# Kernel tuning notes

Hardware: AMD Instinct MI355X
Metric: run time of the kernel (lower is better)

Reference implementation:

```python
import jax, jax.numpy as jnp
import numpy as np

B, C, H, W = 8, 512, 64, 64
S = 64
STD = 0.001  # torch init.normal_(weight, std=0.001)


def setup_inputs() -> dict:
    key = jax.random.key(0)
    ks = jax.random.split(key, 7)
    return {
        "queries": jax.random.normal(ks[0], (B, C, H, W), dtype=jnp.float32),
        "k": jax.random.normal(ks[1], (B, C, H, W), dtype=jnp.float32),
        "v": jax.random.normal(ks[2], (B, C, H, W), dtype=jnp.float32),
        "Wq": jax.random.normal(ks[3], (S, C), dtype=jnp.float32) * STD,
        "Wk": jax.random.normal(ks[4], (S, C), dtype=jnp.float32) * STD,
        "Wv": jax.random.normal(ks[5], (S, C), dtype=jnp.float32) * STD,
        "Wl": jax.random.normal(ks[6], (C, S), dtype=jnp.float32) * STD,
    }


def _branch(A, Bp, Cp, Wl):
    # A,Bp,Cp: [h,w,b,S] projected tensors
    m = jnp.einsum('hwbs,hwbt->hwst', A, Bp)          # [h,w,S,S]
    m = jax.nn.softmax(m, axis=1)                      # softmax over w (dim=1, as in torch)
    o = jnp.einsum('hwst,hwbt->hwsb', m, Cp)           # [h,w,S,b]
    o = o / jnp.sum(o, axis=2, keepdims=True)          # normalize over S
    o = jnp.einsum('hwsb,cs->hwbc', o, Wl)             # transpose + Linear(S->C)
    return jnp.transpose(o, (2, 3, 0, 1))              # [b,c,h,w]


def reference(queries, k, v, Wq, Wk, Wv, Wl):
    q = jnp.transpose(queries, (2, 3, 0, 1))  # [h,w,b,c]
    kk = jnp.transpose(k, (2, 3, 0, 1))
    vv = jnp.transpose(v, (2, 3, 0, 1))
    aq = jnp.einsum('hwbc,sc->hwbs', q, Wq)   # [h,w,b,S]
    ak = jnp.einsum('hwbc,sc->hwbs', kk, Wk)
    av = jnp.einsum('hwbc,sc->hwbs', vv, Wv)
    out_q = _branch(aq, ak, av, Wl)
    out_k = _branch(ak, av, aq, Wl)
    out_v = _branch(av, aq, ak, Wl)
    return jnp.concatenate((out_q, out_k, out_v), axis=0)  # [3b,c,h,w]
```

## Files before the change

kernel.cpp:

```cpp
#include <hip/hip_runtime.h>
#include <hip/hip_bf16.h>

#define HW 4096
#define CCH 512
#define SDIM 64
#define BDIM 8

typedef __attribute__((ext_vector_type(8))) short short8;
typedef __attribute__((ext_vector_type(4))) float f32x4;

static __device__ __forceinline__ ushort f2bf(float f) {
  __hip_bfloat16 h = __float2bfloat16(f);
  return *reinterpret_cast<ushort*>(&h);
}
static __device__ __forceinline__ float bf2f(ushort u) {
  union { unsigned int u32; float f; } c;
  c.u32 = ((unsigned int)u) << 16;
  return c.f;
}

static __device__ __forceinline__ void gll16(const float* g, float* lds_base) {
  __builtin_amdgcn_global_load_lds(
      (const __attribute__((address_space(1))) unsigned int*)g,
      (__attribute__((address_space(3))) unsigned int*)lds_base, 16, 0, 0);
}

__global__ __launch_bounds__(256) void prep_kernel(const float* __restrict__ Wq,
                                                   const float* __restrict__ Wk,
                                                   const float* __restrict__ Wv,
                                                   ushort* __restrict__ whi,
                                                   ushort* __restrict__ wmid,
                                                   ushort* __restrict__ wlo) {
  const float* W = blockIdx.y == 0 ? Wq : (blockIdx.y == 1 ? Wk : Wv);
  const int idx = blockIdx.x * 1024 + threadIdx.x * 4;
  float4 f = *reinterpret_cast<const float4*>(&W[idx]);
  ushort4 h, m, l;
  float r, r2;
  h.x = f2bf(f.x); r = f.x - bf2f(h.x); m.x = f2bf(r); r2 = r - bf2f(m.x); l.x = f2bf(r2);
  h.y = f2bf(f.y); r = f.y - bf2f(h.y); m.y = f2bf(r); r2 = r - bf2f(m.y); l.y = f2bf(r2);
  h.z = f2bf(f.z); r = f.z - bf2f(h.z); m.z = f2bf(r); r2 = r - bf2f(m.z); l.z = f2bf(r2);
  h.w = f2bf(f.w); r = f.w - bf2f(h.w); m.w = f2bf(r); r2 = r - bf2f(m.w); l.w = f2bf(r2);
  const size_t o = (size_t)blockIdx.y * (SDIM * CCH) + idx;
  *reinterpret_cast<ushort4*>(&whi[o])  = h;
  *reinterpret_cast<ushort4*>(&wmid[o]) = m;
  *reinterpret_cast<ushort4*>(&wlo[o])  = l;
}

__global__ __launch_bounds__(256, 2) void proj_mfma_kernel(const float* __restrict__ q,
                                                           const float* __restrict__ k,
                                                           const float* __restrict__ v,
                                                           const ushort* __restrict__ whi,
                                                           const ushort* __restrict__ wmid,
                                                           const ushort* __restrict__ wlo,
                                                           float* __restrict__ ap) {
  __shared__ float Xs[2][4][64 * 32];
  const int mt = blockIdx.x;
  const int b = blockIdx.y;
  const int br = blockIdx.z;
  const float* x = br == 0 ? q : (br == 1 ? k : v);
  const ushort* wh = whi + (size_t)br * SDIM * CCH;
  const ushort* wm = wmid + (size_t)br * SDIM * CCH;
  const ushort* wl = wlo + (size_t)br * SDIM * CCH;
  float* apo = ap + (size_t)br * HW * 512;
  const int hw0 = mt * 128;
  const int tid = threadIdx.x;
  const int l = tid & 63;
  const int wid = tid >> 6;
  const int wstrip = wid * 32;
  const int row16 = l & 15;
  const int kgrp = l >> 4;
  const float* xsrc = x + (size_t)b * CCH * HW + hw0 + wstrip + (l & 7) * 4;
  const int csub = l >> 3;

  f32x4 acc_hi[2][4] = {};
  f32x4 acc_co[2][4] = {};

#define STAGE(BUF, C0)                                                        \
  do {                                                                        \
    float* ldsb = &Xs[BUF][wid][0];                                           \
    _Pragma("unroll") for (int j = 0; j < 8; ++j)                             \
      gll16(xsrc + (size_t)((C0) + j * 8 + csub) * HW, ldsb + j * 256);       \
  } while (0)

#define COMPUTE(BUF, C0)                                                                           \
  do {                                                                                             \
    const float* lw = &Xs[BUF][wid][0];                                                            \
    _Pragma("unroll") for (int ks = 0; ks < 2; ++ks) {                                             \
      short8 bh[4], bm[4], bl[4];                                                                  \
      _Pragma("unroll") for (int nf = 0; nf < 4; ++nf) {                                           \
        const size_t off = (size_t)(nf * 16 + row16) * CCH + (C0) + ks * 32 + kgrp * 8;            \
        bh[nf] = *reinterpret_cast<const short8*>(&wh[off]);                                       \
        bm[nf] = *reinterpret_cast<const short8*>(&wm[off]);                                       \
        bl[nf] = *reinterpret_cast<const short8*>(&wl[off]);                                       \
      }                                                                                            \
      _Pragma("unroll") for (int mf = 0; mf < 2; ++mf) {                                           \
        ushort th[8], tm[8], tl[8];                                                                \
        _Pragma("unroll") for (int i = 0; i < 8; ++i) {                                            \
          const float f = lw[(ks * 32 + kgrp * 8 + i) * 32 + mf * 16 + row16];                     \
          const ushort h = f2bf(f);                                                                \
          const float r = f - bf2f(h);                                                             \
          const ushort mv = f2bf(r);                                                               \
          const float r2 = r - bf2f(mv);                                                           \
          th[i] = h; tm[i] = mv; tl[i] = f2bf(r2);                                                 \
        }                                                                                          \
        const short8 ah = *reinterpret_cast<const short8*>(th);                                    \
        const short8 am = *reinterpret_cast<const short8*>(tm);                                    \
        const short8 al = *reinterpret_cast<const short8*>(tl);                                    \
        _Pragma("unroll") for (int nf = 0; nf < 4; ++nf) {                                         \
          acc_hi[mf][nf] = __builtin_amdgcn_mfma_f32_16x16x32_bf16(ah, bh[nf], acc_hi[mf][nf], 0, 0, 0); \
          acc_co[mf][nf] = __builtin_amdgcn_mfma_f32_16x16x32_bf16(ah, bm[nf], acc_co[mf][nf], 0, 0, 0); \
          acc_co[mf][nf] = __builtin_amdgcn_mfma_f32_16x16x32_bf16(am, bh[nf], acc_co[mf][nf], 0, 0, 0); \
          acc_co[mf][nf] = __builtin_amdgcn_mfma_f32_16x16x32_bf16(am, bm[nf], acc_co[mf][nf], 0, 0, 0); \
          acc_co[mf][nf] = __builtin_amdgcn_mfma_f32_16x16x32_bf16(ah, bl[nf], acc_co[mf][nf], 0, 0, 0); \
          acc_co[mf][nf] = __builtin_amdgcn_mfma_f32_16x16x32_bf16(al, bh[nf], acc_co[mf][nf], 0, 0, 0); \
          acc_co[mf][nf] = __builtin_amdgcn_mfma_f32_16x16x32_bf16(am, bl[nf], acc_co[mf][nf], 0, 0, 0); \
          acc_co[mf][nf] = __builtin_amdgcn_mfma_f32_16x16x32_bf16(al, bm[nf], acc_co[mf][nf], 0, 0, 0); \
        }                                                                                          \
      }                                                                                            \
    }                                                                                              \
  } while (0)

  STAGE(0, 0);
#pragma unroll
  for (int cc = 0; cc < 8; ++cc) {
    if (cc < 7) STAGE((cc + 1) & 1, (cc + 1) * 64);
    __builtin_amdgcn_sched_barrier(0);
    if (cc < 7) {
      asm volatile("s_waitcnt vmcnt(8)" ::: "memory");
    } else {
      asm volatile("s_waitcnt vmcnt(0)" ::: "memory");
    }
    __builtin_amdgcn_sched_barrier(0);
    COMPUTE(cc & 1, cc * 64);
  }
#undef STAGE
#undef COMPUTE

#pragma unroll
  for (int mf = 0; mf < 2; ++mf)
#pragma unroll
    for (int nf = 0; nf < 4; ++nf)
#pragma unroll
      for (int r = 0; r < 4; ++r) {
        const int m = hw0 + wstrip + mf * 16 + kgrp * 4 + r;
        apo[(size_t)m * 512 + b * 64 + nf * 16 + row16] = acc_hi[mf][nf][r] + acc_co[mf][nf][r];
      }
}

__global__ __launch_bounds__(512) void denom_kernel(const float* __restrict__ ap,
                                                    float* __restrict__ rD) {
  __shared__ float As[8 * 16];
  __shared__ float Bs[8 * 64];
  const int h = blockIdx.x, br = blockIdx.y, sq = blockIdx.z;
  const float* A  = ap + ((size_t)br * HW + (size_t)h * 64) * (BDIM * SDIM);
  const float* Bp = ap + ((size_t)((br + 1) % 3) * HW + (size_t)h * 64) * (BDIM * SDIM);
  const int tid = threadIdx.x;
  const int t = tid & 63;
  const int sg = tid >> 6;
  float D[2] = {};
  for (int w = 0; w < 64; ++w) {
    __syncthreads();
    if (tid < 128) As[tid] = A[w * 512 + (tid >> 4) * 64 + sq * 16 + (tid & 15)];
    Bs[tid] = Bp[w * 512 + tid];
    __syncthreads();
    float bv[8];
#pragma unroll
    for (int b = 0; b < 8; ++b) bv[b] = Bs[b * 64 + t];
#pragma unroll
    for (int j = 0; j < 2; ++j) {
      const int sl = sg * 2 + j;
      float m = 0.f;
#pragma unroll
      for (int b = 0; b < 8; ++b) m = fmaf(As[b * 16 + sl], bv[b], m);
      D[j] += __expf(m);
    }
  }
#pragma unroll
  for (int j = 0; j < 2; ++j)
    rD[((size_t)(br * 64 + h) * 64 + sq * 16 + sg * 2 + j) * 64 + t] = 1.0f / D[j];
}

__global__ __launch_bounds__(256) void attn_kernel(const float* __restrict__ ap,
                                                   const float* __restrict__ rD,
                                                   float* __restrict__ on) {
  __shared__ float As[8 * 64], Bs[8 * 64], Cs[8 * 64];
  __shared__ float Ms[64 * 68];
  const int wc = blockIdx.x, h = blockIdx.y, br = blockIdx.z;
  const float* A  = ap + ((size_t)br * HW + h * 64) * 512;
  const float* Bp = ap + ((size_t)((br + 1) % 3) * HW + h * 64) * 512;
  const float* Cp = ap + ((size_t)((br + 2) % 3) * HW + h * 64) * 512;
  const float* rDp = rD + (size_t)(br * 64 + h) * 4096;
  const int tid = threadIdx.x;
  for (int w = wc * 8; w < wc * 8 + 8; ++w) {
    __syncthreads();
#pragma unroll
    for (int it = 0; it < 2; ++it) {
      int idx = it * 256 + tid;
      As[idx] = A[w * 512 + idx];
      Bs[idx] = Bp[w * 512 + idx];
      Cs[idx] = Cp[w * 512 + idx];
    }
    __syncthreads();
    {
      const int t = tid & 63, sg = tid >> 6;
      float bv[8];
#pragma unroll
      for (int b = 0; b < 8; ++b) bv[b] = Bs[b * 64 + t];
#pragma unroll
      for (int j = 0; j < 16; ++j) {
        int s = sg * 16 + j;
        float m = 0.f;
#pragma unroll
        for (int b = 0; b < 8; ++b) m = fmaf(As[b * 64 + s], bv[b], m);
        Ms[s * 68 + t] = __expf(m) * rDp[s * 64 + t];
      }
    }
    __syncthreads();
    const int s2 = tid & 63, bq = tid >> 6;
    float o0 = 0.f, o1 = 0.f;
#pragma unroll
    for (int tt = 0; tt < 64; tt += 4) {
      float4 mv = *reinterpret_cast<const float4*>(&Ms[s2 * 68 + tt]);
      float4 c0 = *reinterpret_cast<const float4*>(&Cs[bq * 64 + tt]);
      float4 c1 = *reinterpret_cast<const float4*>(&Cs[(bq + 4) * 64 + tt]);
      o0 = fmaf(mv.w, c0.w, fmaf(mv.z, c0.z, fmaf(mv.y, c0.y, fmaf(mv.x, c0.x, o0))));
      o1 = fmaf(mv.w, c1.w, fmaf(mv.z, c1.z, fmaf(mv.y, c1.y, fmaf(mv.x, c1.x, o1))));
    }
    float n0 = o0, n1 = o1;
#pragma unroll
    for (int off = 32; off > 0; off >>= 1) {
      n0 += __shfl_xor(n0, off);
      n1 += __shfl_xor(n1, off);
    }
    const float r0 = 1.0f / n0, r1 = 1.0f / n1;
    const size_t ob = ((size_t)br * HW + h * 64 + w) * 512;
    on[ob + (size_t)bq * 64 + s2] = o0 * r0;
    on[ob + (size_t)(bq + 4) * 64 + s2] = o1 * r1;
  }
}

__global__ __launch_bounds__(256) void out_kernel(const float* __restrict__ on,
                                                  const float* __restrict__ wl,
                                                  float* __restrict__ out) {
  __shared__ float Os[128 * 68];
  const int hwt = blockIdx.x;
  const int brb = blockIdx.y;
  const int br = brb >> 3, b = brb & 7;
  const int hw0 = hwt * 128;
  const int tid = threadIdx.x;
  const int l = tid & 63;
  const int wv = tid >> 6;
  const int l15 = l & 15;
  const int kgrp = l >> 4;

  {
    const int row = tid >> 4;
    const int s4 = (tid & 15) * 4;
#pragma unroll
    for (int it = 0; it < 8; ++it) {
      const int r = row + it * 16;
      *reinterpret_cast<float4*>(&Os[r * 68 + s4]) =
          *reinterpret_cast<const float4*>(&on[((size_t)(br * HW + hw0 + r) * 8 + b) * 64 + s4]);
    }
  }
  __syncthreads();

  short8 onh[2][2], onl[2][2];
#pragma unroll
  for (int nf = 0; nf < 2; ++nf)
#pragma unroll
    for (int ks = 0; ks < 2; ++ks) {
      const int row = wv * 32 + nf * 16 + l15;
      const float* p = &Os[row * 68 + ks * 32 + kgrp * 8];
      ushort th[8], tl[8];
#pragma unroll
      for (int i = 0; i < 8; ++i) {
        const float f = p[i];
        const ushort h = f2bf(f);
        th[i] = h;
        tl[i] = f2bf(f - bf2f(h));
      }
      onh[nf][ks] = *reinterpret_cast<const short8*>(th);
      onl[nf][ks] = *reinterpret_cast<const short8*>(tl);
    }

  for (int mf = 0; mf < 32; ++mf) {
    f32x4 acc[2] = {};
#pragma unroll
    for (int ks = 0; ks < 2; ++ks) {
      const float* wp = &wl[(size_t)(mf * 16 + l15) * 64 + ks * 32 + kgrp * 8];
      ushort th[8], tl[8];
#pragma unroll
      for (int i = 0; i < 8; ++i) {
        const float f = wp[i];
        const ushort h = f2bf(f);
        th[i] = h;
        tl[i] = f2bf(f - bf2f(h));
      }
      const short8 wh8 = *reinterpret_cast<const short8*>(th);
      const short8 wl8 = *reinterpret_cast<const short8*>(tl);
#pragma unroll
      for (int nf = 0; nf < 2; ++nf) {
        acc[nf] = __builtin_amdgcn_mfma_f32_16x16x32_bf16(wh8, onh[nf][ks], acc[nf], 0, 0, 0);
        acc[nf] = __builtin_amdgcn_mfma_f32_16x16x32_bf16(wh8, onl[nf][ks], acc[nf], 0, 0, 0);
        acc[nf] = __builtin_amdgcn_mfma_f32_16x16x32_bf16(wl8, onh[nf][ks], acc[nf], 0, 0, 0);
      }
    }
#pragma unroll
    for (int nf = 0; nf < 2; ++nf)
#pragma unroll
      for (int r = 0; r < 4; ++r) {
        const int cc = mf * 16 + kgrp * 4 + r;
        out[(size_t)(brb * 512 + cc) * HW + hw0 + wv * 32 + nf * 16 + l15] = acc[nf][r];
      }
  }
}

extern "C" void kernel_launch(void* const* d_in, const int* in_sizes, int n_in,
                              void* d_out, int out_size, void* d_ws, size_t ws_size,
                              hipStream_t stream) {
  const float* q  = (const float*)d_in[0];
  const float* k  = (const float*)d_in[1];
  const float* v  = (const float*)d_in[2];
  const float* Wq = (const float*)d_in[3];
  const float* Wk = (const float*)d_in[4];
  const float* Wv = (const float*)d_in[5];
  const float* Wl = (const float*)d_in[6];
  float* out = (float*)d_out;

  float* ap = (float*)d_ws;
  float* rD = ap + (size_t)3 * HW * 512;
  float* on = rD + (size_t)3 * 64 * 64 * 64;
  ushort* whi  = (ushort*)rD;
  ushort* wmid = whi + (size_t)3 * SDIM * CCH;
  ushort* wlo  = wmid + (size_t)3 * SDIM * CCH;

  prep_kernel<<<dim3(32, 3), 256, 0, stream>>>(Wq, Wk, Wv, whi, wmid, wlo);
  proj_mfma_kernel<<<dim3(32, 8, 3), 256, 0, stream>>>(q, k, v, whi, wmid, wlo, ap);
  denom_kernel<<<dim3(64, 3, 4), 512, 0, stream>>>(ap, rD);
  attn_kernel<<<dim3(8, 64, 3), 256, 0, stream>>>(ap, rD, on);
  out_kernel<<<dim3(32, 24), 256, 0, stream>>>(on, Wl, out);
}
```

Before: 283.0 us.

## Restructure projection kernel to 512-thread blocks with cooperative 32-channel staging

The projection kernel moves from 256-thread blocks, where each wave privately stages and consumes its own 32-pixel strip in 64-channel chunks, to 512-thread blocks covering 256 pixels. All eight waves now cooperatively load 32-channel slices into a shared double buffer and synchronise with block barriers. Weight fragments are loaded once per 32-channel step rather than per 64-channel chunk. The goal is fewer blocks, coalesced full-row loads and smaller per-wave register and LDS footprints, at the cost of two block-wide barriers per channel step and less latency hiding, since each wave has only one chunk in flight.

Result: slower. 329.3 us (+16.3%).

```diff
diff --git a/kernel.cpp b/kernel.cpp
--- a/kernel.cpp
+++ b/kernel.cpp
@@ -46,14 +46,14 @@
   *reinterpret_cast<ushort4*>(&wlo[o])  = l;
 }
 
-__global__ __launch_bounds__(256, 2) void proj_mfma_kernel(const float* __restrict__ q,
+__global__ __launch_bounds__(512, 2) void proj_mfma_kernel(const float* __restrict__ q,
                                                            const float* __restrict__ k,
                                                            const float* __restrict__ v,
                                                            const ushort* __restrict__ whi,
                                                            const ushort* __restrict__ wmid,
                                                            const ushort* __restrict__ wlo,
                                                            float* __restrict__ ap) {
-  __shared__ float Xs[2][4][64 * 32];
+  __shared__ float Xs[2][32 * 256];
   const int mt = blockIdx.x;
   const int b = blockIdx.y;
   const int br = blockIdx.z;
@@ -62,79 +62,79 @@
   const ushort* wm = wmid + (size_t)br * SDIM * CCH;
   const ushort* wl = wlo + (size_t)br * SDIM * CCH;
   float* apo = ap + (size_t)br * HW * 512;
-  const int hw0 = mt * 128;
+  const int hw0 = mt * 256;
   const int tid = threadIdx.x;
   const int l = tid & 63;
-  const int wid = tid >> 6;
-  const int wstrip = wid * 32;
+  const int w = tid >> 6;
+  const int w4 = w * 4;
   const int row16 = l & 15;
   const int kgrp = l >> 4;
-  const float* xsrc = x + (size_t)b * CCH * HW + hw0 + wstrip + (l & 7) * 4;
-  const int csub = l >> 3;
+  const float* xb = x + (size_t)b * CCH * HW + hw0 + l * 4;
 
   f32x4 acc_hi[2][4] = {};
   f32x4 acc_co[2][4] = {};
 
-#define STAGE(BUF, C0)                                                        \
-  do {                                                                        \
-    float* ldsb = &Xs[BUF][wid][0];                                           \
-    _Pragma("unroll") for (int j = 0; j < 8; ++j)                             \
-      gll16(xsrc + (size_t)((C0) + j * 8 + csub) * HW, ldsb + j * 256);       \
-  } while (0)
-
-#define COMPUTE(BUF, C0)                                                                           \
-  do {                                                                                             \
-    const float* lw = &Xs[BUF][wid][0];                                                            \
-    _Pragma("unroll") for (int ks = 0; ks < 2; ++ks) {                                             \
-      short8 bh[4], bm[4], bl[4];                                                                  \
-      _Pragma("unroll") for (int nf = 0; nf < 4; ++nf) {                                           \
-        const size_t off = (size_t)(nf * 16 + row16) * CCH + (C0) + ks * 32 + kgrp * 8;            \
-        bh[nf] = *reinterpret_cast<const short8*>(&wh[off]);                                       \
-        bm[nf] = *reinterpret_cast<const short8*>(&wm[off]);                                       \
-        bl[nf] = *reinterpret_cast<const short8*>(&wl[off]);                                       \
-      }                                                                                            \
-      _Pragma("unroll") for (int mf = 0; mf < 2; ++mf) {                                           \
-        ushort th[8], tm[8], tl[8];                                                                \
-        _Pragma("unroll") for (int i = 0; i < 8; ++i) {                                            \
-          const float f = lw[(ks * 32 + kgrp * 8 + i) * 32 + mf * 16 + row16];                     \
-          const ushort h = f2bf(f);                                                                \
-          const float r = f - bf2f(h);                                                             \
-          const ushort mv = f2bf(r);                                                               \
-          const float r2 = r - bf2f(mv);                                                           \
-          th[i] = h; tm[i] = mv; tl[i] = f2bf(r2);                                                 \
-        }                                                                                          \
-        const short8 ah = *reinterpret_cast<const short8*>(th);                                    \
-        const short8 am = *reinterpret_cast<const short8*>(tm);                                    \
-        const short8 al = *reinterpret_cast<const short8*>(tl);                                    \
-        _Pragma("unroll") for (int nf = 0; nf < 4; ++nf) {                                         \
-          acc_hi[mf][nf] = __builtin_amdgcn_mfma_f32_16x16x32_bf16(ah, bh[nf], acc_hi[mf][nf], 0, 0, 0); \
-          acc_co[mf][nf] = __builtin_amdgcn_mfma_f32_16x16x32_bf16(ah, bm[nf], acc_co[mf][nf], 0, 0, 0); \
-          acc_co[mf][nf] = __builtin_amdgcn_mfma_f32_16x16x32_bf16(am, bh[nf], acc_co[mf][nf], 0, 0, 0); \
-          acc_co[mf][nf] = __builtin_amdgcn_mfma_f32_16x16x32_bf16(am, bm[nf], acc_co[mf][nf], 0, 0, 0); \
-          acc_co[mf][nf] = __builtin_amdgcn_mfma_f32_16x16x32_bf16(ah, bl[nf], acc_co[mf][nf], 0, 0, 0); \
-          acc_co[mf][nf] = __builtin_amdgcn_mfma_f32_16x16x32_bf16(al, bh[nf], acc_co[mf][nf], 0, 0, 0); \
-          acc_co[mf][nf] = __builtin_amdgcn_mfma_f32_16x16x32_bf16(am, bl[nf], acc_co[mf][nf], 0, 0, 0); \
-          acc_co[mf][nf] = __builtin_amdgcn_mfma_f32_16x16x32_bf16(al, bm[nf], acc_co[mf][nf], 0, 0, 0); \
-        }                                                                                          \
-      }                                                                                            \
-    }                                                                                              \
-  } while (0)
-
-  STAGE(0, 0);
-#pragma unroll
-  for (int cc = 0; cc < 8; ++cc) {
-    if (cc < 7) STAGE((cc + 1) & 1, (cc + 1) * 64);
-    __builtin_amdgcn_sched_barrier(0);
-    if (cc < 7) {
-      asm volatile("s_waitcnt vmcnt(8)" ::: "memory");
+#pragma unroll
+  for (int j = 0; j < 4; ++j)
+    gll16(xb + (size_t)(w4 + j) * HW, &Xs[0][(w4 + j) * 256]);
+
+  for (int ci = 0; ci < 16; ++ci) {
+    short8 bh[4], bm[4], bl[4];
+#pragma unroll
+    for (int nf = 0; nf < 4; ++nf) {
+      const size_t off = (size_t)(nf * 16 + row16) * CCH + ci * 32 + kgrp * 8;
+      bh[nf] = *reinterpret_cast<const short8*>(&wh[off]);
+      bm[nf] = *reinterpret_cast<const short8*>(&wm[off]);
+      bl[nf] = *reinterpret_cast<const short8*>(&wl[off]);
+    }
+    __builtin_amdgcn_sched_barrier(0);
+    if (ci < 15) {
+#pragma unroll
+      for (int j = 0; j < 4; ++j)
+        gll16(xb + (size_t)((ci + 1) * 32 + w4 + j) * HW, &Xs[(ci + 1) & 1][(w4 + j) * 256]);
+    }
+    __builtin_amdgcn_sched_barrier(0);
+    if (ci < 15) {
+      asm volatile("s_waitcnt vmcnt(4)" ::: "memory");
     } else {
       asm volatile("s_waitcnt vmcnt(0)" ::: "memory");
     }
     __builtin_amdgcn_sched_barrier(0);
-    COMPUTE(cc & 1, cc * 64);
-  }
-#undef STAGE
-#undef COMPUTE
+    __builtin_amdgcn_s_barrier();
+    __builtin_amdgcn_sched_barrier(0);
+
+    const float* lw = &Xs[ci & 1][0];
+#pragma unroll
+    for (int mf = 0; mf < 2; ++mf) {
+      ushort th[8], tm[8], tl[8];
+#pragma unroll
+      for (int i = 0; i < 8; ++i) {
+        const float f = lw[(kgrp * 8 + i) * 256 + w * 32 + mf * 16 + row16];
+        const ushort h = f2bf(f);
+        const float r = f - bf2f(h);
+        const ushort mv = f2bf(r);
+        const float r2 = r - bf2f(mv);
+        th[i] = h; tm[i] = mv; tl[i] = f2bf(r2);
+      }
+      const short8 ah = *reinterpret_cast<const short8*>(th);
+      const short8 am = *reinterpret_cast<const short8*>(tm);
+      const short8 al = *reinterpret_cast<const short8*>(tl);
+#pragma unroll
+      for (int nf = 0; nf < 4; ++nf) {
+        acc_hi[mf][nf] = __builtin_amdgcn_mfma_f32_16x16x32_bf16(ah, bh[nf], acc_hi[mf][nf], 0, 0, 0);
+        acc_co[mf][nf] = __builtin_amdgcn_mfma_f32_16x16x32_bf16(ah, bm[nf], acc_co[mf][nf], 0, 0, 0);
+        acc_co[mf][nf] = __builtin_amdgcn_mfma_f32_16x16x32_bf16(am, bh[nf], acc_co[mf][nf], 0, 0, 0);
+        acc_co[mf][nf] = __builtin_amdgcn_mfma_f32_16x16x32_bf16(am, bm[nf], acc_co[mf][nf], 0, 0, 0);
+        acc_co[mf][nf] = __builtin_amdgcn_mfma_f32_16x16x32_bf16(ah, bl[nf], acc_co[mf][nf], 0, 0, 0);
+        acc_co[mf][nf] = __builtin_amdgcn_mfma_f32_16x16x32_bf16(al, bh[nf], acc_co[mf][nf], 0, 0, 0);
+        acc_co[mf][nf] = __builtin_amdgcn_mfma_f32_16x16x32_bf16(am, bl[nf], acc_co[mf][nf], 0, 0, 0);
+        acc_co[mf][nf] = __builtin_amdgcn_mfma_f32_16x16x32_bf16(al, bm[nf], acc_co[mf][nf], 0, 0, 0);
+      }
+    }
+    __builtin_amdgcn_sched_barrier(0);
+    __builtin_amdgcn_s_barrier();
+    __builtin_amdgcn_sched_barrier(0);
+  }
 
 #pragma unroll
   for (int mf = 0; mf < 2; ++mf)
@@ -142,7 +142,7 @@
     for (int nf = 0; nf < 4; ++nf)
 #pragma unroll
       for (int r = 0; r < 4; ++r) {
-        const int m = hw0 + wstrip + mf * 16 + kgrp * 4 + r;
+        const int m = hw0 + w * 32 + mf * 16 + kgrp * 4 + r;
         apo[(size_t)m * 512 + b * 64 + nf * 16 + row16] = acc_hi[mf][nf][r] + acc_co[mf][nf][r];
       }
 }
@@ -336,7 +336,7 @@
   ushort* wlo  = wmid + (size_t)3 * SDIM * CCH;
 
   prep_kernel<<<dim3(32, 3), 256, 0, stream>>>(Wq, Wk, Wv, whi, wmid, wlo);
-  proj_mfma_kernel<<<dim3(32, 8, 3), 256, 0, stream>>>(q, k, v, whi, wmid, wlo, ap);
+  proj_mfma_kernel<<<dim3(16, 8, 3), 512, 0, stream>>>(q, k, v, whi, wmid, wlo, ap);
   denom_kernel<<<dim3(64, 3, 4), 512, 0, stream>>>(ap, rD);
   attn_kernel<<<dim3(8, 64, 3), 256, 0, stream>>>(ap, rD, on);
   out_kernel<<<dim3(32, 24), 256, 0, stream>>>(on, Wl, out);
```
